# Kernel optimization log

Hardware: AMD Instinct MI355X
Metric: run time of the kernel (lower is better)

Reference implementation:

```python
import jax, jax.numpy as jnp
import numpy as np

LMAX = 4
DSH = (LMAX + 1) ** 2          # 25 spherical-harmonic coefficients
C = 32                          # channels per degree l
N = 10000                       # nodes
E = 160000                      # edges
FC = 64                         # fc_len_in (radial/edge scalar feature dim)

# flattened (l,m) index = l^2 + l + m
IDX0 = np.array([l * l + l for l in range(LMAX + 1)])               # m = 0 coeffs
POS = {m: np.array([l * l + l + m for l in range(m, LMAX + 1)]) for m in range(1, LMAX + 1)}
NEG = {m: np.array([l * l + l - m for l in range(m, LMAX + 1)]) for m in range(1, LMAX + 1)}
L_OF_IDX = np.concatenate([np.full(2 * l + 1, l) for l in range(LMAX + 1)])  # degree of each coeff


def setup_inputs() -> dict:
    key = jax.random.key(0)
    ks = jax.random.split(key, 20)
    inp = {
        "x": jax.random.normal(ks[0], (N, DSH, C), jnp.float32),
        "wigner": jax.random.normal(ks[1], (E, DSH, DSH), jnp.float32) * 0.2,
        "edge_fc": jax.random.normal(ks[2], (E, FC), jnp.float32),
        "edge_src": jax.random.randint(ks[3], (E,), 0, N),
        "edge_dst": jax.random.randint(ks[4], (E,), 0, N),
    }
    # per-m SO(2) block weights
    d0 = (LMAX + 1) * C
    inp["w0"] = jax.random.normal(ks[5], (d0, d0), jnp.float32) / np.sqrt(d0)
    k = 6
    for m in range(1, LMAX + 1):
        dm = (LMAX + 1 - m) * C
        inp[f"w{m}r"] = jax.random.normal(ks[k], (dm, dm), jnp.float32) / np.sqrt(dm); k += 1
        inp[f"w{m}i"] = jax.random.normal(ks[k], (dm, dm), jnp.float32) / np.sqrt(dm); k += 1
    # radial/cfconv network producing per-(degree, channel) scales
    inp["fc_w"] = jax.random.normal(ks[k], (FC, (LMAX + 1) * C), jnp.float32) / np.sqrt(FC)
    inp["fc_b"] = jnp.zeros(((LMAX + 1) * C,), jnp.float32)
    return inp


def reference(x, wigner, edge_fc, edge_src, edge_dst,
              w0, w1r, w1i, w2r, w2i, w3r, w3i, w4r, w4i, fc_w, fc_b):
    Wr = {1: w1r, 2: w2r, 3: w3r, 4: w4r}
    Wi = {1: w1i, 2: w2i, 3: w3i, 4: w4i}
    # gather node features to edges and rotate into edge-aligned frame
    xe = x[edge_src]                                   # [E, 25, C]
    xr = jnp.einsum('eij,ejc->eic', wigner, xe)        # [E, 25, C]
    Ee = xr.shape[0]
    y = jnp.zeros_like(xr)
    # m = 0 block: real linear over stacked-l channels
    x0 = xr[:, IDX0, :].reshape(Ee, -1)                # [E, 5*C]
    y = y.at[:, IDX0, :].set((x0 @ w0).reshape(Ee, LMAX + 1, C))
    # m > 0 blocks: SO(2) complex-style mixing
    for m in range(1, LMAX + 1):
        pos, neg = POS[m], NEG[m]
        Lm = len(pos)
        xp = xr[:, pos, :].reshape(Ee, -1)             # [E, Lm*C]
        xn = xr[:, neg, :].reshape(Ee, -1)
        yp = xp @ Wr[m] - xn @ Wi[m]
        yn = xp @ Wi[m] + xn @ Wr[m]
        y = y.at[:, pos, :].set(yp.reshape(Ee, Lm, C))
        y = y.at[:, neg, :].set(yn.reshape(Ee, Lm, C))
    # cfconv: per-edge radial scaling, one scalar per (degree, channel)
    scale = jax.nn.silu(edge_fc @ fc_w + fc_b).reshape(Ee, LMAX + 1, C)
    y = y * scale[:, L_OF_IDX, :]
    # rotate back (Wigner D is orthogonal -> transpose is inverse)
    yb = jnp.einsum('eji,ejc->eic', wigner, y)
    # scatter-aggregate messages to destination nodes
    return jax.ops.segment_sum(yb, edge_dst, num_segments=N)
```

## Files before the change

kernel.cpp:

```cpp
#include <hip/hip_runtime.h>

typedef __attribute__((ext_vector_type(8))) short short8;
typedef __attribute__((ext_vector_type(4))) short short4v;
typedef __attribute__((ext_vector_type(4))) float f32x4;

#define MFMA16(a,b,c) __builtin_amdgcn_mfma_f32_16x16x32_bf16((a),(b),(c),0,0,0)

__device__ __align__(16) short g_wt[117760];
__device__ __align__(16) short g_wtf[148480];
__device__ __align__(16) short g_fcwt[10240];

struct K2Tab {
  int   fbase[50];
  int   pboff[50][8];
  short acoeff[50][8];
  short len[50];
  short dm[50];
  short ut[50];
  short ocoeff[50];
  short lsc[50];
  short co16[50];
  short pu[290];
  short pk[290];
};

constexpr K2Tab make_k2tab() {
  K2Tab T{};
  const int P[5][5]  = {{0,2,6,12,20},{3,7,13,21,0},{8,14,22,0,0},{15,23,0,0,0},{24,0,0,0,0}};
  const int Ng[5][5] = {{0,0,0,0,0},{1,5,11,19,0},{4,10,18,0,0},{9,17,0,0,0},{16,0,0,0,0}};
  const int WR[5]  = {0, 25600, 74752, 102400, 114688};
  const int WI[5]  = {0, 41984, 83968, 106496, 115712};
  const int NWI[5] = {0, 58368, 93184, 110592, 116736};
  const int ms[9]  = {1,1,2,2,0,3,3,4,4};
  const int hs[9]  = {0,1,0,1,0,0,1,0,1};
  const int ntc[9] = {8,8,6,6,10,4,4,2,2};
  int u = 0, fb = 0, np = 0;
  for (int g = 0; g < 9; ++g) {
    const int m = ms[g], h = hs[g];
    const int dm = (m == 0) ? 160 : (5 - m) * 32;
    const int lm = (m == 0) ? 5 : (5 - m);
    const int len = (m == 0) ? 5 : 2 * lm;
    const int b1 = (m == 0) ? 0 : ((h == 0) ? WR[m] : WI[m]);
    const int b2 = (m == 0) ? 0 : ((h == 0) ? NWI[m] : WR[m]);
    for (int tt = 0; tt < ntc[g]; ++tt, ++u) {
      T.dm[u] = (short)dm; T.len[u] = (short)len; T.ut[u] = (short)tt;
      const int lo = tt >> 1;
      T.ocoeff[u] = (short)((m == 0) ? P[0][lo] : ((h == 0) ? P[m][lo] : Ng[m][lo]));
      T.lsc[u] = (short)(m + lo);
      T.co16[u] = (short)((tt & 1) * 16);
      T.fbase[u] = fb;
      for (int k = 0; k < len; ++k) {
        int bb, ac;
        if (m == 0)      { bb = k * 32;            ac = P[0][k]; }
        else if (k < lm) { bb = b1 + k * 32;       ac = P[m][k]; }
        else             { bb = b2 + (k - lm) * 32; ac = Ng[m][k - lm]; }
        T.pboff[u][k] = bb; T.acoeff[u][k] = (short)ac;
        T.pu[np] = (short)u; T.pk[np] = (short)k; ++np;
      }
      fb += len * 512;
    }
  }
  return T;
}
__constant__ K2Tab c_kt = make_k2tab();

__device__ __forceinline__ short f2bf(float f) {
  unsigned u = __float_as_uint(f);
  u += 0x7FFFu + ((u >> 16) & 1u);
  return (short)(u >> 16);
}

__global__ void prep_weights(const float* __restrict__ w0,
    const float* __restrict__ w1r, const float* __restrict__ w1i,
    const float* __restrict__ w2r, const float* __restrict__ w2i,
    const float* __restrict__ w3r, const float* __restrict__ w3i,
    const float* __restrict__ w4r, const float* __restrict__ w4i,
    const float* __restrict__ fcw) {
  int idx = blockIdx.x * 256 + threadIdx.x;
  if (idx >= 128000) return;
  if (idx >= 117760) {
    int local = idx - 117760;
    int n = local >> 6, k = local & 63;
    g_fcwt[local] = f2bf(fcw[k * 160 + n]);
    return;
  }
  int off, dm; const float* src; bool neg = false;
  if (idx < 25600)       { off = 0;      dm = 160; src = w0;  }
  else if (idx < 41984)  { off = 25600;  dm = 128; src = w1r; }
  else if (idx < 58368)  { off = 41984;  dm = 128; src = w1i; }
  else if (idx < 74752)  { off = 58368;  dm = 128; src = w1i; neg = true; }
  else if (idx < 83968)  { off = 74752;  dm = 96;  src = w2r; }
  else if (idx < 93184)  { off = 83968;  dm = 96;  src = w2i; }
  else if (idx < 102400) { off = 93184;  dm = 96;  src = w2i; neg = true; }
  else if (idx < 106496) { off = 102400; dm = 64;  src = w3r; }
  else if (idx < 110592) { off = 106496; dm = 64;  src = w3i; }
  else if (idx < 114688) { off = 110592; dm = 64;  src = w3i; neg = true; }
  else if (idx < 115712) { off = 114688; dm = 32;  src = w4r; }
  else if (idx < 116736) { off = 115712; dm = 32;  src = w4i; }
  else                   { off = 116736; dm = 32;  src = w4i; neg = true; }
  int local = idx - off;
  int n = local / dm, k = local - n * dm;
  float v = src[k * dm + n];
  g_wt[idx] = f2bf(neg ? -v : v);
}

__global__ void prep_frags() {
  int i = blockIdx.x * 256 + threadIdx.x;
  if (i >= 290 * 512) return;
  int p = i >> 9;
  int w = i & 511;
  int lane = w >> 3, j = w & 7;
  int l15 = lane & 15, lg = lane >> 4;
  int u = c_kt.pu[p], k = c_kt.pk[p];
  int col = (int)c_kt.ut[u] * 16 + l15;
  g_wtf[i] = g_wt[c_kt.pboff[u][k] + col * (int)c_kt.dm[u] + lg * 8 + j];
}

__global__ void hist_kernel(const int* __restrict__ edst, int* __restrict__ cnt, int E) {
  int i = blockIdx.x * 256 + threadIdx.x;
  if (i < E) atomicAdd(&cnt[edst[i]], 1);
}

__global__ __launch_bounds__(1024) void scan_kernel(
    const int* __restrict__ cnt, int* __restrict__ cursor, int N) {
  __shared__ int s[1024];
  const int t = threadIdx.x;
  int v[10]; int sum = 0;
  #pragma unroll
  for (int k = 0; k < 10; ++k) {
    int i = t * 10 + k;
    v[k] = (i < N) ? cnt[i] : 0;
    sum += v[k];
  }
  s[t] = sum;
  __syncthreads();
  for (int d = 1; d < 1024; d <<= 1) {
    int add = (t >= d) ? s[t - d] : 0;
    __syncthreads();
    s[t] += add;
    __syncthreads();
  }
  int prefix = s[t] - sum;
  #pragma unroll
  for (int k = 0; k < 10; ++k) {
    int i = t * 10 + k;
    if (i < N) cursor[i] = prefix;
    prefix += v[k];
  }
}

__global__ void scatter_kernel(const int* __restrict__ edst, int* __restrict__ cursor,
                               int* __restrict__ order, int E) {
  int i = blockIdx.x * 256 + threadIdx.x;
  if (i < E) {
    int p = atomicAdd(&cursor[edst[i]], 1);
    order[p] = i;
  }
}

#define ESTRIDE 1048
#define YSTRIDE 1024
#define SMEM_ALL 72144

__global__ __launch_bounds__(512, 4) void k_all(
    const float* __restrict__ x, const float* __restrict__ wig,
    const float* __restrict__ efc, const int* __restrict__ esrc,
    const int* __restrict__ edst, const int* __restrict__ order,
    const float* __restrict__ fcb, const int* __restrict__ cnt,
    float* __restrict__ out, int E)
{
  extern __shared__ char smem[];
  short*    s_buf  = (short*)smem;
  short*    s_y    = (short*)(smem + 33536);
  _Float16* s_sc   = (_Float16*)(smem + 66304);
  int*      s_meta = (int*)(smem + 71680);
  float*    yb_s   = (float*)smem;

  const int tid = threadIdx.x;
  const int lane = tid & 63;
  const int wid = tid >> 6;
  const int l15 = lane & 15;
  const int lg  = lane >> 4;
  const int koff = lg * 8;
  const int e0  = blockIdx.x * 16;

  for (int o = tid; o < 1792; o += 512) {
    int e = o / 112, q = o - e * 112;
    ((int*)s_buf)[e * 524 + 400 + q] = 0;
  }
  for (int o = tid; o < 1792; o += 512) {
    int e = o / 112, q = o - e * 112;
    ((int*)s_y)[e * 512 + 400 + q] = 0;
  }
  if (tid < 16) {
    int idx = e0 + tid;
    bool v = idx < E;
    int og = order[v ? idx : 0];
    s_meta[tid] = og;
    s_meta[16 + tid] = esrc[og];
    s_meta[32 + tid] = v ? edst[og] : -1;
  }
  __syncthreads();

  if (wid == 0) {
    int dj = (lane < 16) ? s_meta[32 + lane] : -1;
    bool valid = (lane < 16) && (dj >= 0);
    bool is_start = valid && (lane == 0 || dj != s_meta[32 + lane - 1]);
    unsigned long long vm = __ballot(valid);
    unsigned long long sm = __ballot(is_start);
    int nv = __popcll(vm);
    int ng = __popcll(sm);
    if (lane == 0) s_meta[48] = ng;
    if ((int)lane < ng) {
      int s = -1, c = -1;
      for (int b = 0; b < 16; ++b) { if ((sm >> b) & 1) { ++c; if (c == (int)lane) { s = b; break; } } }
      int e_ = nv;
      for (int b = s + 1; b < 16; ++b) if ((sm >> b) & 1) { e_ = b; break; }
      int d = s_meta[32 + s];
      s_meta[49 + lane] = d;
      s_meta[65 + lane] = s;
      s_meta[81 + lane] = e_;
      s_meta[97 + lane] = ((e_ - s) == cnt[d]) ? 1 : 0;
    }
  }

  for (int o = tid; o < 12800; o += 512) {
    int e = o / 800, q = o - e * 800;
    s_buf[e * ESTRIDE + q] = f2bf(x[(size_t)s_meta[16 + e] * 800 + q]);
  }
  {
    const int ge = s_meta[l15];
    const float* ep = efc + (size_t)ge * 64;
    float4 fa = *(const float4*)(ep + lg * 8);
    float4 fb = *(const float4*)(ep + lg * 8 + 4);
    float4 fc = *(const float4*)(ep + 32 + lg * 8);
    float4 fd = *(const float4*)(ep + 32 + lg * 8 + 4);
    short8 af0, af1;
    af0[0]=f2bf(fa.x); af0[1]=f2bf(fa.y); af0[2]=f2bf(fa.z); af0[3]=f2bf(fa.w);
    af0[4]=f2bf(fb.x); af0[5]=f2bf(fb.y); af0[6]=f2bf(fb.z); af0[7]=f2bf(fb.w);
    af1[0]=f2bf(fc.x); af1[1]=f2bf(fc.y); af1[2]=f2bf(fc.z); af1[3]=f2bf(fc.w);
    af1[4]=f2bf(fd.x); af1[5]=f2bf(fd.y); af1[6]=f2bf(fd.z); af1[7]=f2bf(fd.w);
    for (int nt = wid; nt < 10; nt += 8) {
      const int f = nt * 16 + l15;
      const short* bp = g_fcwt + f * 64 + lg * 8;
      short8 b0 = *(const short8*)(bp);
      short8 b1 = *(const short8*)(bp + 32);
      f32x4 acc = {0.f, 0.f, 0.f, 0.f};
      acc = MFMA16(af0, b0, acc);
      acc = MFMA16(af1, b1, acc);
      float bias = fcb[f];
      #pragma unroll
      for (int r = 0; r < 4; ++r) {
        float vv = acc[r] + bias;
        s_sc[(lg * 4 + r) * 168 + (f >> 5) * 33 + (f & 31)] =
            (_Float16)(vv / (1.f + __expf(-vv)));
      }
    }
  }
  __syncthreads();

  #pragma unroll 2
  for (int i = 0; i < 2; ++i) {
    const int e = wid * 2 + i;
    short* eb = s_buf + e * ESTRIDE;
    const float* wp = wig + (size_t)s_meta[e] * 625;
    short8 a0, a1;
    #pragma unroll
    for (int j = 0; j < 8; ++j) {
      const int k = koff + j;
      a0[j] = eb[k * 32 + l15];
      a1[j] = eb[k * 32 + 16 + l15];
    }
    short8 b0, b1;
    const int r1 = min(16 + l15, 24);
    #pragma unroll
    for (int j = 0; j < 8; ++j) {
      const int k = koff + j;
      const int kc = min(k, 24);
      const short v0 = f2bf(wp[l15 * 25 + kc]);
      const short v1 = f2bf(wp[r1 * 25 + kc]);
      b0[j] = (k < 25) ? v0 : (short)0;
      b1[j] = (k < 25) ? v1 : (short)0;
    }
    f32x4 d00 = {0.f,0.f,0.f,0.f}, d01 = {0.f,0.f,0.f,0.f};
    f32x4 d10 = {0.f,0.f,0.f,0.f}, d11 = {0.f,0.f,0.f,0.f};
    d00 = MFMA16(a0, b0, d00);
    d01 = MFMA16(a0, b1, d01);
    d10 = MFMA16(a1, b0, d10);
    d11 = MFMA16(a1, b1, d11);
    short4v v;
    v[0]=f2bf(d00[0]); v[1]=f2bf(d00[1]); v[2]=f2bf(d00[2]); v[3]=f2bf(d00[3]);
    *(short4v*)(eb + l15 * 32 + lg * 4) = v;
    v[0]=f2bf(d10[0]); v[1]=f2bf(d10[1]); v[2]=f2bf(d10[2]); v[3]=f2bf(d10[3]);
    *(short4v*)(eb + l15 * 32 + 16 + lg * 4) = v;
    if (l15 < 9) {
      v[0]=f2bf(d01[0]); v[1]=f2bf(d01[1]); v[2]=f2bf(d01[2]); v[3]=f2bf(d01[3]);
      *(short4v*)(eb + (16 + l15) * 32 + lg * 4) = v;
      v[0]=f2bf(d11[0]); v[1]=f2bf(d11[1]); v[2]=f2bf(d11[2]); v[3]=f2bf(d11[3]);
      *(short4v*)(eb + (16 + l15) * 32 + 16 + lg * 4) = v;
    }
  }
  __syncthreads();

  for (int u = wid; u < 50; u += 8) {
    const int len = c_kt.len[u];
    const short* Bp = g_wtf + c_kt.fbase[u] + lane * 8;
    short8 B[8];
    #pragma unroll 8
    for (int k = 0; k < 8; ++k)
      if (k < len) B[k] = *(const short8*)(Bp + (k << 9));
    const int co = c_kt.co16[u] + l15;
    const int oc = c_kt.ocoeff[u];
    const int ls = c_kt.lsc[u];
    const short* xl = s_buf + l15 * ESTRIDE + koff;
    f32x4 acc0 = {0.f,0.f,0.f,0.f}, acc1 = {0.f,0.f,0.f,0.f};
    #pragma unroll 8
    for (int k = 0; k < 8; ++k) {
      if (k < len) {
        short8 a = *(const short8*)(xl + (int)c_kt.acoeff[u][k] * 32);
        if (k & 1) acc1 = MFMA16(a, B[k], acc1);
        else       acc0 = MFMA16(a, B[k], acc0);
      }
    }
    f32x4 acc = acc0 + acc1;
    #pragma unroll
    for (int r = 0; r < 4; ++r) {
      const int el = lg * 4 + r;
      float sc = (float)s_sc[el * 168 + ls * 33 + co];
      s_y[el * YSTRIDE + oc * 32 + co] = f2bf(acc[r] * sc);
    }
  }
  __syncthreads();

  f32x4 r00[2], r01[2], r10[2], r11[2];
  #pragma unroll 2
  for (int i = 0; i < 2; ++i) {
    const int e = wid * 2 + i;
    const short* yb = s_y + e * YSTRIDE;
    const float* wp = wig + (size_t)s_meta[e] * 625;
    short8 a0, a1, b0, b1;
    const int c2 = min(16 + l15, 24);
    #pragma unroll 8
    for (int j = 0; j < 8; ++j) {
      const int k = koff + j;
      a0[j] = yb[k * 32 + l15];
      a1[j] = yb[k * 32 + 16 + l15];
      const int kc = min(k, 24);
      const short v0 = f2bf(wp[kc * 25 + l15]);
      const short v1 = f2bf(wp[kc * 25 + c2]);
      b0[j] = (k < 25) ? v0 : (short)0;
      b1[j] = (k < 25) ? v1 : (short)0;
    }
    f32x4 d00 = {0.f,0.f,0.f,0.f}, d01 = {0.f,0.f,0.f,0.f};
    f32x4 d10 = {0.f,0.f,0.f,0.f}, d11 = {0.f,0.f,0.f,0.f};
    d00 = MFMA16(a0, b0, d00);
    d01 = MFMA16(a0, b1, d01);
    d10 = MFMA16(a1, b0, d10);
    d11 = MFMA16(a1, b1, d11);
    r00[i] = d00; r01[i] = d01; r10[i] = d10; r11[i] = d11;
  }
  __syncthreads();

  #pragma unroll 2
  for (int i = 0; i < 2; ++i) {
    const int e = wid * 2 + i;
    float* yb = yb_s + e * 840;
    #pragma unroll 4
    for (int r = 0; r < 4; ++r) {
      yb[l15 * 33 + lg * 4 + r]      = r00[i][r];
      yb[l15 * 33 + 16 + lg * 4 + r] = r10[i][r];
    }
    if (l15 < 9) {
      #pragma unroll 4
      for (int r = 0; r < 4; ++r) {
        yb[(16 + l15) * 33 + lg * 4 + r]      = r01[i][r];
        yb[(16 + l15) * 33 + 16 + lg * 4 + r] = r11[i][r];
      }
    }
  }
  __syncthreads();

  const int ng = s_meta[48];
  for (int o = tid; o < 800; o += 512) {
    const int yoff = (o >> 5) * 33 + (o & 31);
    for (int g = 0; g < ng; ++g) {
      float sum = 0.f;
      const int gs = s_meta[65 + g], ge = s_meta[81 + g];
      for (int e = gs; e < ge; ++e) sum += yb_s[e * 840 + yoff];
      float* ad = out + (size_t)s_meta[49 + g] * 800 + o;
      if (s_meta[97 + g]) *ad = sum;
      else atomicAdd(ad, sum);
    }
  }
}

extern "C" void kernel_launch(void* const* d_in, const int* in_sizes, int n_in,
                              void* d_out, int out_size, void* d_ws, size_t ws_size,
                              hipStream_t stream) {
  const float* x    = (const float*)d_in[0];
  const float* wigp = (const float*)d_in[1];
  const float* efc  = (const float*)d_in[2];
  const int*   esrc = (const int*)d_in[3];
  const int*   edst = (const int*)d_in[4];
  const float* w0   = (const float*)d_in[5];
  const float* w1r  = (const float*)d_in[6];
  const float* w1i  = (const float*)d_in[7];
  const float* w2r  = (const float*)d_in[8];
  const float* w2i  = (const float*)d_in[9];
  const float* w3r  = (const float*)d_in[10];
  const float* w3i  = (const float*)d_in[11];
  const float* w4r  = (const float*)d_in[12];
  const float* w4i  = (const float*)d_in[13];
  const float* fcw  = (const float*)d_in[14];
  const float* fcb  = (const float*)d_in[15];
  float* out = (float*)d_out;
  const int E = in_sizes[3];
  const int N = out_size / 800;

  int* cnt    = (int*)d_ws;
  int* cursor = cnt + N;
  int* order  = cnt + 2 * N;

  hipFuncSetAttribute((const void*)k_all,
                      hipFuncAttributeMaxDynamicSharedMemorySize, SMEM_ALL);

  prep_weights<<<(128000 + 255) / 256, 256, 0, stream>>>(
      w0, w1r, w1i, w2r, w2i, w3r, w3i, w4r, w4i, fcw);
  prep_frags<<<(290 * 512 + 255) / 256, 256, 0, stream>>>();

  hipMemsetAsync(d_out, 0, (size_t)out_size * sizeof(float), stream);
  hipMemsetAsync(cnt, 0, (size_t)N * sizeof(int), stream);

  hist_kernel<<<(E + 255) / 256, 256, 0, stream>>>(edst, cnt, E);
  scan_kernel<<<1, 1024, 0, stream>>>(cnt, cursor, N);
  scatter_kernel<<<(E + 255) / 256, 256, 0, stream>>>(edst, cursor, order, E);

  k_all<<<(E + 15) / 16, 512, SMEM_ALL, stream>>>(
      x, wigp, efc, esrc, edst, order, fcb, cnt, out, E);
}
```

Before: 704.2 us.

## Double block size to 1024 threads with one wave per edge

The fused edge kernel now launches 1024-thread blocks, so each of the 16 waves handles one edge instead of two. The per-wave two-edge loops in the rotation, back-rotation and store phases collapse to single iterations. The fc, SO(2) and scatter loops are re-strided to match. The goal is more waves per CU to hide memory and LDS latency under the same 72 KB LDS footprint. The tighter launch bounds (1024, 8) cap registers per thread and may cause spills in the B-fragment-heavy SO(2) stage.

```diff
diff --git a/kernel.cpp b/kernel.cpp
--- a/kernel.cpp
+++ b/kernel.cpp
@@ -162,7 +162,7 @@
 #define YSTRIDE 1024
 #define SMEM_ALL 72144
 
-__global__ __launch_bounds__(512, 4) void k_all(
+__global__ __launch_bounds__(1024, 8) void k_all(
     const float* __restrict__ x, const float* __restrict__ wig,
     const float* __restrict__ efc, const int* __restrict__ esrc,
     const int* __restrict__ edst, const int* __restrict__ order,
@@ -184,11 +184,11 @@
   const int koff = lg * 8;
   const int e0  = blockIdx.x * 16;
 
-  for (int o = tid; o < 1792; o += 512) {
+  for (int o = tid; o < 1792; o += 1024) {
     int e = o / 112, q = o - e * 112;
     ((int*)s_buf)[e * 524 + 400 + q] = 0;
   }
-  for (int o = tid; o < 1792; o += 512) {
+  for (int o = tid; o < 1792; o += 1024) {
     int e = o / 112, q = o - e * 112;
     ((int*)s_y)[e * 512 + 400 + q] = 0;
   }
@@ -224,11 +224,13 @@
     }
   }
 
-  for (int o = tid; o < 12800; o += 512) {
-    int e = o / 800, q = o - e * 800;
-    s_buf[e * ESTRIDE + q] = f2bf(x[(size_t)s_meta[16 + e] * 800 + q]);
-  }
-  {
+  for (int o = tid; o < 12800; o += 1024) {
+    int e = o >> 3, q = o & 7;
+    (void)e; (void)q;
+    int ee = o / 800, qq = o - ee * 800;
+    s_buf[ee * ESTRIDE + qq] = f2bf(x[(size_t)s_meta[16 + ee] * 800 + qq]);
+  }
+  if (wid < 10) {
     const int ge = s_meta[l15];
     const float* ep = efc + (size_t)ge * 64;
     float4 fa = *(const float4*)(ep + lg * 8);
@@ -240,28 +242,26 @@
     af0[4]=f2bf(fb.x); af0[5]=f2bf(fb.y); af0[6]=f2bf(fb.z); af0[7]=f2bf(fb.w);
     af1[0]=f2bf(fc.x); af1[1]=f2bf(fc.y); af1[2]=f2bf(fc.z); af1[3]=f2bf(fc.w);
     af1[4]=f2bf(fd.x); af1[5]=f2bf(fd.y); af1[6]=f2bf(fd.z); af1[7]=f2bf(fd.w);
-    for (int nt = wid; nt < 10; nt += 8) {
-      const int f = nt * 16 + l15;
-      const short* bp = g_fcwt + f * 64 + lg * 8;
-      short8 b0 = *(const short8*)(bp);
-      short8 b1 = *(const short8*)(bp + 32);
-      f32x4 acc = {0.f, 0.f, 0.f, 0.f};
-      acc = MFMA16(af0, b0, acc);
-      acc = MFMA16(af1, b1, acc);
-      float bias = fcb[f];
-      #pragma unroll
-      for (int r = 0; r < 4; ++r) {
-        float vv = acc[r] + bias;
-        s_sc[(lg * 4 + r) * 168 + (f >> 5) * 33 + (f & 31)] =
-            (_Float16)(vv / (1.f + __expf(-vv)));
-      }
-    }
-  }
-  __syncthreads();
-
-  #pragma unroll 2
-  for (int i = 0; i < 2; ++i) {
-    const int e = wid * 2 + i;
+    const int nt = wid;
+    const int f = nt * 16 + l15;
+    const short* bp = g_fcwt + f * 64 + lg * 8;
+    short8 b0 = *(const short8*)(bp);
+    short8 b1 = *(const short8*)(bp + 32);
+    f32x4 acc = {0.f, 0.f, 0.f, 0.f};
+    acc = MFMA16(af0, b0, acc);
+    acc = MFMA16(af1, b1, acc);
+    float bias = fcb[f];
+    #pragma unroll
+    for (int r = 0; r < 4; ++r) {
+      float vv = acc[r] + bias;
+      s_sc[(lg * 4 + r) * 168 + (f >> 5) * 33 + (f & 31)] =
+          (_Float16)(vv / (1.f + __expf(-vv)));
+    }
+  }
+  __syncthreads();
+
+  {
+    const int e = wid;
     short* eb = s_buf + e * ESTRIDE;
     const float* wp = wig + (size_t)s_meta[e] * 625;
     short8 a0, a1;
@@ -302,7 +302,7 @@
   }
   __syncthreads();
 
-  for (int u = wid; u < 50; u += 8) {
+  for (int u = wid; u < 50; u += 16) {
     const int len = c_kt.len[u];
     const short* Bp = g_wtf + c_kt.fbase[u] + lane * 8;
     short8 B[8];
@@ -332,10 +332,9 @@
   }
   __syncthreads();
 
-  f32x4 r00[2], r01[2], r10[2], r11[2];
-  #pragma unroll 2
-  for (int i = 0; i < 2; ++i) {
-    const int e = wid * 2 + i;
+  f32x4 r00, r01, r10, r11;
+  {
+    const int e = wid;
     const short* yb = s_y + e * YSTRIDE;
     const float* wp = wig + (size_t)s_meta[e] * 625;
     short8 a0, a1, b0, b1;
@@ -357,31 +356,31 @@
     d01 = MFMA16(a0, b1, d01);
     d10 = MFMA16(a1, b0, d10);
     d11 = MFMA16(a1, b1, d11);
-    r00[i] = d00; r01[i] = d01; r10[i] = d10; r11[i] = d11;
-  }
-  __syncthreads();
-
-  #pragma unroll 2
-  for (int i = 0; i < 2; ++i) {
-    const int e = wid * 2 + i;
+    r00 = d00; r01 = d01; r10 = d10; r11 = d11;
+  }
+  __syncthreads();
+
+  {
+    const int e = wid;
     float* yb = yb_s + e * 840;
     #pragma unroll 4
     for (int r = 0; r < 4; ++r) {
-      yb[l15 * 33 + lg * 4 + r]      = r00[i][r];
-      yb[l15 * 33 + 16 + lg * 4 + r] = r10[i][r];
+      yb[l15 * 33 + lg * 4 + r]      = r00[r];
+      yb[l15 * 33 + 16 + lg * 4 + r] = r10[r];
     }
     if (l15 < 9) {
       #pragma unroll 4
       for (int r = 0; r < 4; ++r) {
-        yb[(16 + l15) * 33 + lg * 4 + r]      = r01[i][r];
-        yb[(16 + l15) * 33 + 16 + lg * 4 + r] = r11[i][r];
+        yb[(16 + l15) * 33 + lg * 4 + r]      = r01[r];
+        yb[(16 + l15) * 33 + 16 + lg * 4 + r] = r11[r];
       }
     }
   }
   __syncthreads();
 
   const int ng = s_meta[48];
-  for (int o = tid; o < 800; o += 512) {
+  if (tid < 800) {
+    const int o = tid;
     const int yoff = (o >> 5) * 33 + (o & 31);
     for (int g = 0; g < ng; ++g) {
       float sum = 0.f;
@@ -435,6 +434,6 @@
   scan_kernel<<<1, 1024, 0, stream>>>(cnt, cursor, N);
   scatter_kernel<<<(E + 255) / 256, 256, 0, stream>>>(edst, cursor, order, E);
 
-  k_all<<<(E + 15) / 16, 512, SMEM_ALL, stream>>>(
+  k_all<<<(E + 15) / 16, 1024, SMEM_ALL, stream>>>(
       x, wigp, efc, esrc, edst, order, fcb, cnt, out, E);
 }
```

After: 1.060 ms. +50.5%, slower.

## Move radial scale computation to separate kernel and shrink LDS for occupancy

Applied to the files above, without the earlier changes.

Computes the per-edge SiLU radial scales in a new standalone kernel that writes bf16 scales to workspace in sorted-edge order, removing the in-kernel MFMA scale path and its LDS buffer. The main kernel's shared memory shrinks (unpadded strides, with padding rows replaced by clamped masked loads) and launch bounds rise to allow more resident blocks. The trade-off is an extra kernel that does scalar fp32 FMAs, plus a global round-trip of E*160 bf16 values that the main kernel reads back.

```diff
diff --git a/kernel.cpp b/kernel.cpp
--- a/kernel.cpp
+++ b/kernel.cpp
@@ -8,7 +8,6 @@
 
 __device__ __align__(16) short g_wt[117760];
 __device__ __align__(16) short g_wtf[148480];
-__device__ __align__(16) short g_fcwt[10240];
 
 struct K2Tab {
   int   fbase[50];
@@ -69,21 +68,17 @@
   u += 0x7FFFu + ((u >> 16) & 1u);
   return (short)(u >> 16);
 }
+__device__ __forceinline__ float bf2f(short s) {
+  return __uint_as_float(((unsigned)(unsigned short)s) << 16);
+}
 
 __global__ void prep_weights(const float* __restrict__ w0,
     const float* __restrict__ w1r, const float* __restrict__ w1i,
     const float* __restrict__ w2r, const float* __restrict__ w2i,
     const float* __restrict__ w3r, const float* __restrict__ w3i,
-    const float* __restrict__ w4r, const float* __restrict__ w4i,
-    const float* __restrict__ fcw) {
+    const float* __restrict__ w4r, const float* __restrict__ w4i) {
   int idx = blockIdx.x * 256 + threadIdx.x;
-  if (idx >= 128000) return;
-  if (idx >= 117760) {
-    int local = idx - 117760;
-    int n = local >> 6, k = local & 63;
-    g_fcwt[local] = f2bf(fcw[k * 160 + n]);
-    return;
-  }
+  if (idx >= 117760) return;
   int off, dm; const float* src; bool neg = false;
   if (idx < 25600)       { off = 0;      dm = 160; src = w0;  }
   else if (idx < 41984)  { off = 25600;  dm = 128; src = w1r; }
@@ -158,23 +153,34 @@
   }
 }
 
-#define ESTRIDE 1048
-#define YSTRIDE 1024
-#define SMEM_ALL 72144
-
-__global__ __launch_bounds__(512, 4) void k_all(
+__global__ void k_scales(const float* __restrict__ efc, const int* __restrict__ order,
+                         const float* __restrict__ fcw, const float* __restrict__ fcb,
+                         short* __restrict__ scg, int E) {
+  int i = blockIdx.x * 256 + threadIdx.x;
+  if (i >= E * 160) return;
+  int slot = i / 160, f = i - slot * 160;
+  const float* ep = efc + (size_t)order[slot] * 64;
+  float a = fcb[f];
+  #pragma unroll 8
+  for (int k = 0; k < 64; ++k) a = fmaf(ep[k], fcw[k * 160 + f], a);
+  scg[i] = f2bf(a / (1.f + __expf(-a)));
+}
+
+#define ESTRIDE 800
+#define YBSTRIDE 824
+#define SMEM_ALL 53200
+
+__global__ __launch_bounds__(512, 6) void k_all(
     const float* __restrict__ x, const float* __restrict__ wig,
-    const float* __restrict__ efc, const int* __restrict__ esrc,
-    const int* __restrict__ edst, const int* __restrict__ order,
-    const float* __restrict__ fcb, const int* __restrict__ cnt,
-    float* __restrict__ out, int E)
+    const int* __restrict__ esrc, const int* __restrict__ edst,
+    const int* __restrict__ order, const int* __restrict__ cnt,
+    const short* __restrict__ scg, float* __restrict__ out, int E)
 {
   extern __shared__ char smem[];
-  short*    s_buf  = (short*)smem;
-  short*    s_y    = (short*)(smem + 33536);
-  _Float16* s_sc   = (_Float16*)(smem + 66304);
-  int*      s_meta = (int*)(smem + 71680);
-  float*    yb_s   = (float*)smem;
+  short* s_buf  = (short*)smem;
+  short* s_y    = (short*)(smem + 25600);
+  int*   s_meta = (int*)(smem + 52736);
+  float* yb_s   = (float*)smem;
 
   const int tid = threadIdx.x;
   const int lane = tid & 63;
@@ -184,14 +190,6 @@
   const int koff = lg * 8;
   const int e0  = blockIdx.x * 16;
 
-  for (int o = tid; o < 1792; o += 512) {
-    int e = o / 112, q = o - e * 112;
-    ((int*)s_buf)[e * 524 + 400 + q] = 0;
-  }
-  for (int o = tid; o < 1792; o += 512) {
-    int e = o / 112, q = o - e * 112;
-    ((int*)s_y)[e * 512 + 400 + q] = 0;
-  }
   if (tid < 16) {
     int idx = e0 + tid;
     bool v = idx < E;
@@ -225,37 +223,8 @@
   }
 
   for (int o = tid; o < 12800; o += 512) {
-    int e = o / 800, q = o - e * 800;
-    s_buf[e * ESTRIDE + q] = f2bf(x[(size_t)s_meta[16 + e] * 800 + q]);
-  }
-  {
-    const int ge = s_meta[l15];
-    const float* ep = efc + (size_t)ge * 64;
-    float4 fa = *(const float4*)(ep + lg * 8);
-    float4 fb = *(const float4*)(ep + lg * 8 + 4);
-    float4 fc = *(const float4*)(ep + 32 + lg * 8);
-    float4 fd = *(const float4*)(ep + 32 + lg * 8 + 4);
-    short8 af0, af1;
-    af0[0]=f2bf(fa.x); af0[1]=f2bf(fa.y); af0[2]=f2bf(fa.z); af0[3]=f2bf(fa.w);
-    af0[4]=f2bf(fb.x); af0[5]=f2bf(fb.y); af0[6]=f2bf(fb.z); af0[7]=f2bf(fb.w);
-    af1[0]=f2bf(fc.x); af1[1]=f2bf(fc.y); af1[2]=f2bf(fc.z); af1[3]=f2bf(fc.w);
-    af1[4]=f2bf(fd.x); af1[5]=f2bf(fd.y); af1[6]=f2bf(fd.z); af1[7]=f2bf(fd.w);
-    for (int nt = wid; nt < 10; nt += 8) {
-      const int f = nt * 16 + l15;
-      const short* bp = g_fcwt + f * 64 + lg * 8;
-      short8 b0 = *(const short8*)(bp);
-      short8 b1 = *(const short8*)(bp + 32);
-      f32x4 acc = {0.f, 0.f, 0.f, 0.f};
-      acc = MFMA16(af0, b0, acc);
-      acc = MFMA16(af1, b1, acc);
-      float bias = fcb[f];
-      #pragma unroll
-      for (int r = 0; r < 4; ++r) {
-        float vv = acc[r] + bias;
-        s_sc[(lg * 4 + r) * 168 + (f >> 5) * 33 + (f & 31)] =
-            (_Float16)(vv / (1.f + __expf(-vv)));
-      }
-    }
+    int ee = o / 800, qq = o - ee * 800;
+    s_buf[ee * ESTRIDE + qq] = f2bf(x[(size_t)s_meta[16 + ee] * 800 + qq]);
   }
   __syncthreads();
 
@@ -268,8 +237,11 @@
     #pragma unroll
     for (int j = 0; j < 8; ++j) {
       const int k = koff + j;
-      a0[j] = eb[k * 32 + l15];
-      a1[j] = eb[k * 32 + 16 + l15];
+      const int kc = min(k, 24);
+      const short u0 = eb[kc * 32 + l15];
+      const short u1 = eb[kc * 32 + 16 + l15];
+      a0[j] = (k < 25) ? u0 : (short)0;
+      a1[j] = (k < 25) ? u1 : (short)0;
     }
     short8 b0, b1;
     const int r1 = min(16 + l15, 24);
@@ -326,8 +298,9 @@
     #pragma unroll
     for (int r = 0; r < 4; ++r) {
       const int el = lg * 4 + r;
-      float sc = (float)s_sc[el * 168 + ls * 33 + co];
-      s_y[el * YSTRIDE + oc * 32 + co] = f2bf(acc[r] * sc);
+      const int sl = min(e0 + el, E - 1);
+      float sc = bf2f(scg[(size_t)sl * 160 + ls * 32 + co]);
+      s_y[el * ESTRIDE + oc * 32 + co] = f2bf(acc[r] * sc);
     }
   }
   __syncthreads();
@@ -336,16 +309,18 @@
   #pragma unroll 2
   for (int i = 0; i < 2; ++i) {
     const int e = wid * 2 + i;
-    const short* yb = s_y + e * YSTRIDE;
+    const short* yb = s_y + e * ESTRIDE;
     const float* wp = wig + (size_t)s_meta[e] * 625;
     short8 a0, a1, b0, b1;
     const int c2 = min(16 + l15, 24);
     #pragma unroll 8
     for (int j = 0; j < 8; ++j) {
       const int k = koff + j;
-      a0[j] = yb[k * 32 + l15];
-      a1[j] = yb[k * 32 + 16 + l15];
       const int kc = min(k, 24);
+      const short u0 = yb[kc * 32 + l15];
+      const short u1 = yb[kc * 32 + 16 + l15];
+      a0[j] = (k < 25) ? u0 : (short)0;
+      a1[j] = (k < 25) ? u1 : (short)0;
       const short v0 = f2bf(wp[kc * 25 + l15]);
       const short v1 = f2bf(wp[kc * 25 + c2]);
       b0[j] = (k < 25) ? v0 : (short)0;
@@ -364,7 +339,7 @@
   #pragma unroll 2
   for (int i = 0; i < 2; ++i) {
     const int e = wid * 2 + i;
-    float* yb = yb_s + e * 840;
+    float* yb = yb_s + e * YBSTRIDE;
     #pragma unroll 4
     for (int r = 0; r < 4; ++r) {
       yb[l15 * 33 + lg * 4 + r]      = r00[i][r];
@@ -386,7 +361,7 @@
     for (int g = 0; g < ng; ++g) {
       float sum = 0.f;
       const int gs = s_meta[65 + g], ge = s_meta[81 + g];
-      for (int e = gs; e < ge; ++e) sum += yb_s[e * 840 + yoff];
+      for (int e = gs; e < ge; ++e) sum += yb_s[e * YBSTRIDE + yoff];
       float* ad = out + (size_t)s_meta[49 + g] * 800 + o;
       if (s_meta[97 + g]) *ad = sum;
       else atomicAdd(ad, sum);
@@ -420,12 +395,14 @@
   int* cnt    = (int*)d_ws;
   int* cursor = cnt + N;
   int* order  = cnt + 2 * N;
+  size_t sc_off = (((size_t)(2 * N + E) * 4) + 255) & ~(size_t)255;
+  short* scg = (short*)((char*)d_ws + sc_off);
 
   hipFuncSetAttribute((const void*)k_all,
                       hipFuncAttributeMaxDynamicSharedMemorySize, SMEM_ALL);
 
-  prep_weights<<<(128000 + 255) / 256, 256, 0, stream>>>(
-      w0, w1r, w1i, w2r, w2i, w3r, w3i, w4r, w4i, fcw);
+  prep_weights<<<(117760 + 255) / 256, 256, 0, stream>>>(
+      w0, w1r, w1i, w2r, w2i, w3r, w3i, w4r, w4i);
   prep_frags<<<(290 * 512 + 255) / 256, 256, 0, stream>>>();
 
   hipMemsetAsync(d_out, 0, (size_t)out_size * sizeof(float), stream);
@@ -434,7 +411,8 @@
   hist_kernel<<<(E + 255) / 256, 256, 0, stream>>>(edst, cnt, E);
   scan_kernel<<<1, 1024, 0, stream>>>(cnt, cursor, N);
   scatter_kernel<<<(E + 255) / 256, 256, 0, stream>>>(edst, cursor, order, E);
+  k_scales<<<(E * 160 + 255) / 256, 256, 0, stream>>>(efc, order, fcw, fcb, scg, E);
 
   k_all<<<(E + 15) / 16, 512, SMEM_ALL, stream>>>(
-      x, wigp, efc, esrc, edst, order, fcb, cnt, out, E);
-}
+      x, wigp, esrc, edst, order, cnt, scg, out, E);
+}
```

After: 1.030 ms. 46.3% more time.
